# Optimization experiments

Measured on AMD Instinct MI355X. Metric: run time of the kernel, lower is better.

Reference implementation:

```python
import jax, jax.numpy as jnp
import numpy as np

B, T, D, H = 4, 2048, 1024, 16
HD = D // H  # head_dim = 64


def setup_inputs() -> dict:
    key = jax.random.key(0)
    k1, k2, k3 = jax.random.split(key, 3)
    s = 0.02
    return {
        "x": jax.random.normal(k1, (B, T, D), dtype=jnp.float32),
        "qkv_w": jax.random.normal(k2, (D, 3 * D), dtype=jnp.float32) * s,
        "qkv_b": jnp.zeros((3 * D,), dtype=jnp.float32),
        "proj_w": jax.random.normal(k3, (D, D), dtype=jnp.float32) * s,
        "proj_b": jnp.zeros((D,), dtype=jnp.float32),
    }


def reference(x, qkv_w, qkv_b, proj_w, proj_b):
    b, t, d = x.shape
    qkv = x @ qkv_w + qkv_b                       # [B,T,3D]
    q, k, v = jnp.split(qkv, 3, axis=-1)
    # [B,T,D] -> [B,H,T,hd]
    q = q.reshape(b, t, H, HD).transpose(0, 2, 1, 3)
    k = k.reshape(b, t, H, HD).transpose(0, 2, 1, 3)
    v = v.reshape(b, t, H, HD).transpose(0, 2, 1, 3)
    att = jnp.einsum("bhqd,bhkd->bhqk", q, k) / np.sqrt(HD).astype(np.float32)
    causal = jnp.tril(jnp.ones((t, t), dtype=bool))
    att = jnp.where(causal[None, None], att, jnp.finfo(att.dtype).min)
    att = jax.nn.softmax(att, axis=-1)
    out = jnp.einsum("bhqk,bhkd->bhqd", att, v)   # [B,H,T,hd]
    out = out.transpose(0, 2, 1, 3).reshape(b, t, H * HD)
    out = out @ proj_w + proj_b                   # dropout p=0.0 -> identity
    return out
```

## Files before the change

### kernel.cpp

```cpp
#include <hip/hip_runtime.h>
#include <hip/hip_bf16.h>

#define Bsz 4
#define Tsz 2048
#define Dsz 1024
#define Hsz 16
#define HDsz 64

typedef __attribute__((ext_vector_type(8))) __bf16 bf16x8;
typedef __attribute__((ext_vector_type(4))) __bf16 bf16x4;
typedef __attribute__((ext_vector_type(4))) float f32x4;
typedef __attribute__((ext_vector_type(2))) float f32x2;
typedef unsigned short u16;
typedef unsigned int u32;

#define DEVI static __device__ __forceinline__

DEVI u16 f2bf(float f) {
    __bf16 h = (__bf16)f;
    union { __bf16 h; u16 u; } c; c.h = h; return c.u;
}
DEVI bf16x8 ld_bf8(const u16* p) { return *reinterpret_cast<const bf16x8*>(p); }

DEVI void gll16(const u16* g, u16* lds) {
    __builtin_amdgcn_global_load_lds(
        (const __attribute__((address_space(1))) u32*)g,
        (__attribute__((address_space(3))) u32*)lds, 16, 0, 0);
}

DEVI void mfma16(f32x4& c, f32x2 a, f32x2 b) {
    asm("v_mfma_f32_16x16x16_bf16 %0, %1, %2, %0" : "+v"(c) : "v"(a), "v"(b));
}

__global__ __launch_bounds__(256)
void conv_bf16(const float* __restrict__ X, u16* __restrict__ Xb)
{
    const size_t i = ((size_t)blockIdx.x * 256 + threadIdx.x) * 8;
    const float4 a = *(const float4*)(X + i);
    const float4 b = *(const float4*)(X + i + 4);
    u16 h[8] = { f2bf(a.x), f2bf(a.y), f2bf(a.z), f2bf(a.w),
                 f2bf(b.x), f2bf(b.y), f2bf(b.z), f2bf(b.w) };
    *(uint4*)(Xb + i) = *(uint4*)h;
}

__global__ __launch_bounds__(256)
void transpose_w(const float* __restrict__ W, u16* __restrict__ WT, int K, int N)
{
    __shared__ float tile[64][65];
    const int n0 = blockIdx.x * 64, k0 = blockIdx.y * 64;
    const int t = threadIdx.x;
    #pragma unroll
    for (int i = 0; i < 4; ++i) {
        const int idx = i*256 + t;
        const int row = idx >> 4, c4 = (idx & 15) * 4;
        const float4 v = *(const float4*)(W + (size_t)(k0 + row)*N + n0 + c4);
        tile[row][c4+0] = v.x; tile[row][c4+1] = v.y;
        tile[row][c4+2] = v.z; tile[row][c4+3] = v.w;
    }
    __syncthreads();
    #pragma unroll
    for (int j = 0; j < 2; ++j) {
        const int idx = j*256 + t;
        const int nr = idx >> 3, kc = (idx & 7) * 8;
        u16 h[8];
        #pragma unroll
        for (int e = 0; e < 8; ++e) h[e] = f2bf(tile[kc + e][nr]);
        *(uint4*)(WT + (size_t)(n0 + nr)*K + k0 + kc) = *(uint4*)h;
    }
}

template<int EPI>
__global__ __launch_bounds__(256, 3)
void gemm128(const u16* __restrict__ A, const u16* __restrict__ Bt,
             const float* __restrict__ bias, float* __restrict__ Cf,
             u16* __restrict__ Qo, u16* __restrict__ Ko, u16* __restrict__ Vo,
             int M, int N, int K)
{
    __shared__ u16 As[3][128][32];
    __shared__ u16 Bs[3][128][32];

    const int nx  = N >> 7;
    const int q   = nx >> 3;
    const int xcd = blockIdx.x & 7;
    const int c   = blockIdx.x >> 3;
    const int tN  = xcd * q + (q > 1 ? (c % q) : 0);
    const int tM  = (q > 1 ? (c / q) : c);

    const int t = threadIdx.x, l = t & 63, w = t >> 6;
    const int wm = w >> 1, wn = w & 1;
    const int lrow = l & 15, lk = l >> 4;

    f32x4 acc[4][4] = {};

    const u16* Ag = A  + (size_t)tM * 128 * K;
    const u16* Bg = Bt + (size_t)tN * 128 * K;

    int srow[2], sch[2];
    #pragma unroll
    for (int r = 0; r < 2; ++r) {
        const int cc = r*256 + t;
        srow[r] = cc >> 2;
        sch[r]  = (cc & 3) ^ ((srow[r] >> 1) & 3);
    }
    const size_t ldso = (size_t)(t & 192) * 8;

    #define STAGE(buf, ks)                                                      \
        {                                                                       \
            _Pragma("unroll")                                                   \
            for (int r = 0; r < 2; ++r) {                                       \
                gll16(Ag + (size_t)srow[r]*K + (ks) + sch[r]*8,                 \
                      &As[buf][0][0] + (size_t)r*2048 + ldso);                  \
                gll16(Bg + (size_t)srow[r]*K + (ks) + sch[r]*8,                 \
                      &Bs[buf][0][0] + (size_t)r*2048 + ldso);                  \
            }                                                                   \
        }

    STAGE(0, 0);
    STAGE(1, 32);

    const int nk = K >> 5;
    int cur = 0;
    for (int i = 0; i < nk; ++i) {
        if (i + 1 < nk) { asm volatile("s_waitcnt vmcnt(4)" ::: "memory"); }
        else            { asm volatile("s_waitcnt vmcnt(0)" ::: "memory"); }
        __builtin_amdgcn_sched_barrier(0);
        __builtin_amdgcn_s_barrier();

        bf16x8 a[4], bb[4];
        #pragma unroll
        for (int ii = 0; ii < 4; ++ii) {
            const int ar = wm*64 + ii*16 + lrow;
            a[ii] = ld_bf8(&As[cur][ar][(lk ^ ((ar >> 1) & 3)) * 8]);
        }
        #pragma unroll
        for (int j = 0; j < 4; ++j) {
            const int br = wn*64 + j*16 + lrow;
            bb[j] = ld_bf8(&Bs[cur][br][(lk ^ ((br >> 1) & 3)) * 8]);
        }

        if (i + 2 < nk) {
            const int nb = (cur + 2) - ((cur + 2) >= 3 ? 3 : 0);
            STAGE(nb, (i + 2) * 32);
        }

        __builtin_amdgcn_s_setprio(1);
        #pragma unroll
        for (int ii = 0; ii < 4; ++ii)
        #pragma unroll
        for (int j = 0; j < 4; ++j)
            acc[ii][j] = __builtin_amdgcn_mfma_f32_16x16x32_bf16(a[ii], bb[j], acc[ii][j], 0, 0, 0);
        __builtin_amdgcn_s_setprio(0);

        cur = (cur + 1) - ((cur + 1) >= 3 ? 3 : 0);
    }
    #undef STAGE

    #pragma unroll
    for (int i = 0; i < 4; ++i)
    #pragma unroll
    for (int j = 0; j < 4; ++j) {
        const int row0 = tM*128 + wm*64 + i*16 + lk*4;
        const int col  = tN*128 + wn*64 + j*16 + lrow;
        const float bv = bias[col];
        if (EPI == 0) {
            #pragma unroll
            for (int r = 0; r < 4; ++r)
                Cf[(size_t)(row0 + r) * N + col] = acc[i][j][r] + bv;
        } else {
            const int which = col >> 10;
            const int h  = (col & 1023) >> 6;
            const int hd = col & 63;
            if (which == 2) {
                const int b  = row0 >> 11;
                const int tt = row0 & 2047;
                const int bh = b * Hsz + h;
                u16 pk[4] = { f2bf(acc[i][j][0] + bv), f2bf(acc[i][j][1] + bv),
                              f2bf(acc[i][j][2] + bv), f2bf(acc[i][j][3] + bv) };
                *(ushort4*)(Vo + ((size_t)bh * HDsz + hd) * Tsz + tt) = *(ushort4*)pk;
            } else {
                u16* P = (which == 0) ? Qo : Ko;
                #pragma unroll
                for (int r = 0; r < 4; ++r) {
                    const int row = row0 + r;
                    const int bh  = (row >> 11) * Hsz + h;
                    P[((size_t)bh * Tsz + (row & 2047)) * HDsz + hd] =
                        f2bf(acc[i][j][r] + bv);
                }
            }
        }
    }
}

__global__ __launch_bounds__(256, 4)
void attn3(const u16* __restrict__ Q, const u16* __restrict__ K,
           const u16* __restrict__ Vt, u16* __restrict__ AO)
{
    __shared__ u16 KV[2][2][64][64];

    const int y = blockIdx.y;
    const int x = blockIdx.x;
    const int idx = (x + (y >> 4)) & 15;
    const int qt = (idx & 1) ? (idx >> 1) : (15 - (idx >> 1));
    const int bh = y;
    const int t = threadIdx.x, w = t >> 6, l = t & 63;
    const int lrow = l & 15, lk = l >> 4;
    const int qw = qt*128 + w*32;
    const int qwmax = qw + 31;
    const int swz = lrow & 7;

    const u16* Qh = Q  + (size_t)bh * Tsz * HDsz;
    const u16* Kh = K  + (size_t)bh * Tsz * HDsz;
    const u16* Vh = Vt + (size_t)bh * HDsz * Tsz;

    bf16x8 qf[2][2];
    #pragma unroll
    for (int f = 0; f < 2; ++f)
    #pragma unroll
    for (int kh = 0; kh < 2; ++kh)
        qf[f][kh] = ld_bf8(&Qh[(size_t)(qw + f*16 + lrow)*HDsz + kh*32 + lk*8]);

    f32x4 o[2][4] = {};
    float m[2] = {-3e38f, -3e38f}, lsum[2] = {0.f, 0.f};

    const int ntile = 2*qt + 2;
    int cur = 0;

    #pragma unroll
    for (int rr = 0; rr < 2; ++rr) {
        const int c = rr*256 + t;
        const int row = c >> 3, gc = (c & 7) ^ (row & 7);
        gll16(Kh + (size_t)row*HDsz + gc*8,
              &KV[0][0][0][0] + (size_t)(rr*256 + (t & 192))*8);
        gll16(Vh + (size_t)row*Tsz + gc*8,
              &KV[0][1][0][0] + (size_t)(rr*256 + (t & 192))*8);
    }
    __syncthreads();

    for (int tk = 0; tk < ntile; ++tk) {
        if (tk + 1 < ntile) {
            const int nkv = (tk + 1) * 64;
            #pragma unroll
            for (int rr = 0; rr < 2; ++rr) {
                const int c = rr*256 + t;
                const int row = c >> 3, gc = (c & 7) ^ (row & 7);
                gll16(Kh + (size_t)(nkv + row)*HDsz + gc*8,
                      &KV[cur^1][0][0][0] + (size_t)(rr*256 + (t & 192))*8);
                gll16(Vh + (size_t)row*Tsz + nkv + gc*8,
                      &KV[cur^1][1][0][0] + (size_t)(rr*256 + (t & 192))*8);
            }
        }
        const int kv0 = tk * 64;
        if (kv0 <= qwmax) {
            const u16 (*Ks)[64] = KV[cur][0];
            const u16 (*Vs)[64] = KV[cur][1];
            const bool fullc    = (kv0 + 63 <= qwmax);
            const bool needmask = (kv0 + 63 > qw);

            f32x4 s[2][4];
            __builtin_amdgcn_s_setprio(1);
            #pragma unroll
            for (int c = 0; c < 4; ++c) {
                if (c >= 2 && !fullc) continue;
                const bf16x8 k0 = ld_bf8(&Ks[c*16 + lrow][((0 + lk) ^ swz) * 8]);
                const bf16x8 k1 = ld_bf8(&Ks[c*16 + lrow][((4 + lk) ^ swz) * 8]);
                #pragma unroll
                for (int f = 0; f < 2; ++f) {
                    f32x4 z = {};
                    z = __builtin_amdgcn_mfma_f32_16x16x32_bf16(k0, qf[f][0], z, 0, 0, 0);
                    z = __builtin_amdgcn_mfma_f32_16x16x32_bf16(k1, qf[f][1], z, 0, 0, 0);
                    s[f][c] = z;
                }
            }
            __builtin_amdgcn_s_setprio(0);

            #pragma unroll
            for (int f = 0; f < 2; ++f) {
                const int q = qw + f*16 + lrow;
                if (needmask) {
                    #pragma unroll
                    for (int c = 0; c < 4; ++c) {
                        if (c >= 2 && !fullc) continue;
                        const int base = kv0 + c*16 + lk*4;
                        #pragma unroll
                        for (int r = 0; r < 4; ++r)
                            if (base + r > q) s[f][c][r] = -1e30f;
                    }
                }
                f32x4 t01;
                #pragma unroll
                for (int r = 0; r < 4; ++r) {
                    t01[r] = fmaxf(s[f][0][r], s[f][1][r]);
                    if (fullc) t01[r] = fmaxf(t01[r], fmaxf(s[f][2][r], s[f][3][r]));
                }
                float mx = fmaxf(fmaxf(t01[0], t01[1]), fmaxf(t01[2], t01[3]));
                mx = fmaxf(mx, __shfl_xor(mx, 16));
                mx = fmaxf(mx, __shfl_xor(mx, 32));
                if (__any(mx > m[f] + 64.f)) {
                    const float mn = fmaxf(m[f], mx);
                    const float al = __expf((m[f] - mn) * 0.125f);
                    lsum[f] *= al;
                    m[f] = mn;
                    #pragma unroll
                    for (int c = 0; c < 4; ++c)
                    #pragma unroll
                    for (int r = 0; r < 4; ++r) o[f][c][r] *= al;
                }
                const float nm8 = -m[f] * 0.125f;
                f32x4 ps4 = {};
                #pragma unroll
                for (int c = 0; c < 4; ++c) {
                    if (c >= 2 && !fullc) continue;
                    #pragma unroll
                    for (int r = 0; r < 4; ++r) {
                        const float p = __expf(fmaf(s[f][c][r], 0.125f, nm8));
                        s[f][c][r] = p;
                        ps4[r] += p;
                    }
                }
                float ps = (ps4[0] + ps4[1]) + (ps4[2] + ps4[3]);
                ps += __shfl_xor(ps, 16);
                ps += __shfl_xor(ps, 32);
                lsum[f] += ps;
            }

            __builtin_amdgcn_s_setprio(1);
            #pragma unroll
            for (int c = 0; c < 4; ++c) {
                if (c >= 2 && !fullc) continue;
                union { bf16x4 v; f32x2 f; } p0, p1;
                #pragma unroll
                for (int r = 0; r < 4; ++r) {
                    p0.v[r] = (__bf16)s[0][c][r];
                    p1.v[r] = (__bf16)s[1][c][r];
                }
                #pragma unroll
                for (int chd = 0; chd < 4; ++chd) {
                    const f32x2 va = *reinterpret_cast<const f32x2*>(
                        &Vs[chd*16 + lrow][(((c*2 + (lk >> 1)) ^ swz) << 3) + ((lk & 1) << 2)]);
                    mfma16(o[0][chd], va, p0.f);
                    mfma16(o[1][chd], va, p1.f);
                }
            }
            __builtin_amdgcn_s_setprio(0);
        }
        __syncthreads();
        cur ^= 1;
    }

    const int b = bh >> 4, h = bh & 15;
    #pragma unroll
    for (int f = 0; f < 2; ++f) {
        const float rl = 1.0f / lsum[f];
        #pragma unroll
        for (int chd = 0; chd < 4; ++chd) {
            u16 ov[4] = { f2bf(o[f][chd][0]*rl), f2bf(o[f][chd][1]*rl),
                          f2bf(o[f][chd][2]*rl), f2bf(o[f][chd][3]*rl) };
            *(ushort4*)(AO + ((size_t)(b*Tsz + qw + f*16 + lrow))*Dsz
                           + h*HDsz + chd*16 + lk*4) = *(ushort4*)ov;
        }
    }
}

extern "C" void kernel_launch(void* const* d_in, const int* in_sizes, int n_in,
                              void* d_out, int out_size, void* d_ws, size_t ws_size,
                              hipStream_t stream)
{
    (void)in_sizes; (void)n_in; (void)out_size; (void)ws_size;

    const float* x      = (const float*)d_in[0];
    const float* qkv_w  = (const float*)d_in[1];
    const float* qkv_b  = (const float*)d_in[2];
    const float* proj_w = (const float*)d_in[3];
    const float* proj_b = (const float*)d_in[4];
    float* out = (float*)d_out;

    char* ws = (char*)d_ws;
    const size_t SZ = (size_t)Bsz * Hsz * Tsz * HDsz * sizeof(u16);
    u16* R0 = (u16*)(ws);
    u16* Qb = (u16*)(ws + SZ);
    u16* Kb = (u16*)(ws + 2*SZ);
    u16* Vt = (u16*)(ws + 3*SZ);
    u16* WQKVT = R0;
    u16* AO    = R0;
    u16* WPT   = Qb;

    u16* Xb = (u16*)d_out;

    const int M = Bsz * Tsz;

    conv_bf16<<<(M*Dsz)/(256*8), 256, 0, stream>>>(x, Xb);
    transpose_w<<<dim3(3*Dsz/64, Dsz/64), 256, 0, stream>>>(qkv_w, WQKVT, Dsz, 3*Dsz);
    gemm128<1><<<dim3((3*Dsz/128) * (M/128)), 256, 0, stream>>>(
        Xb, WQKVT, qkv_b, nullptr, Qb, Kb, Vt, M, 3*Dsz, Dsz);
    attn3<<<dim3(Tsz/128, Bsz*Hsz), 256, 0, stream>>>(Qb, Kb, Vt, AO);
    transpose_w<<<dim3(Dsz/64, Dsz/64), 256, 0, stream>>>(proj_w, WPT, Dsz, Dsz);
    gemm128<0><<<dim3((Dsz/128) * (M/128)), 256, 0, stream>>>(
        AO, WPT, proj_b, out, nullptr, nullptr, nullptr, M, Dsz, Dsz);
}
```

Baseline: 194.4 us.

## Triple-buffer K/V tiles in attention with one barrier per iteration

The attention kernel moves from a double-buffered K/V LDS ring to a triple-buffered one, prefetching two tiles ahead. It waits with explicit vmcnt counters and takes a single barrier per iteration in place of the trailing __syncthreads. The goal is to hide global-load latency and cut synchronisation stalls. In exchange LDS use per block grows from 32 KB to 48 KB and the occupancy hint drops from 4 to 3 blocks per CU. Correctness now depends on hand-counted vmcnt values matching the number of outstanding loads.

```diff
diff --git a/kernel.cpp b/kernel.cpp
--- a/kernel.cpp
+++ b/kernel.cpp
@@ -191,11 +191,11 @@
     }
 }
 
-__global__ __launch_bounds__(256, 4)
-void attn3(const u16* __restrict__ Q, const u16* __restrict__ K,
+__global__ __launch_bounds__(256, 3)
+void attn6(const u16* __restrict__ Q, const u16* __restrict__ K,
            const u16* __restrict__ Vt, u16* __restrict__ AO)
 {
-    __shared__ u16 KV[2][2][64][64];
+    __shared__ u16 KV[3][2][64][64];
 
     const int y = blockIdx.y;
     const int x = blockIdx.x;
@@ -218,37 +218,42 @@
     #pragma unroll
     for (int kh = 0; kh < 2; ++kh)
         qf[f][kh] = ld_bf8(&Qh[(size_t)(qw + f*16 + lrow)*HDsz + kh*32 + lk*8]);
+    asm volatile("s_waitcnt vmcnt(0)" ::: "memory");
 
     f32x4 o[2][4] = {};
     float m[2] = {-3e38f, -3e38f}, lsum[2] = {0.f, 0.f};
 
     const int ntile = 2*qt + 2;
+
+    #define AST(buf, tkv)                                                       \
+        {                                                                       \
+            const int nkv_ = (tkv) * 64;                                        \
+            _Pragma("unroll")                                                   \
+            for (int rr = 0; rr < 2; ++rr) {                                    \
+                const int c_ = rr*256 + t;                                      \
+                const int row_ = c_ >> 3, gc_ = (c_ & 7) ^ (row_ & 7);          \
+                gll16(Kh + (size_t)(nkv_ + row_)*HDsz + gc_*8,                  \
+                      &KV[buf][0][0][0] + (size_t)(rr*256 + (t & 192))*8);      \
+                gll16(Vh + (size_t)row_*Tsz + nkv_ + gc_*8,                     \
+                      &KV[buf][1][0][0] + (size_t)(rr*256 + (t & 192))*8);      \
+            }                                                                   \
+        }
+
+    AST(0, 0)
+    AST(1, 1)
+
     int cur = 0;
-
-    #pragma unroll
-    for (int rr = 0; rr < 2; ++rr) {
-        const int c = rr*256 + t;
-        const int row = c >> 3, gc = (c & 7) ^ (row & 7);
-        gll16(Kh + (size_t)row*HDsz + gc*8,
-              &KV[0][0][0][0] + (size_t)(rr*256 + (t & 192))*8);
-        gll16(Vh + (size_t)row*Tsz + gc*8,
-              &KV[0][1][0][0] + (size_t)(rr*256 + (t & 192))*8);
-    }
-    __syncthreads();
-
     for (int tk = 0; tk < ntile; ++tk) {
-        if (tk + 1 < ntile) {
-            const int nkv = (tk + 1) * 64;
-            #pragma unroll
-            for (int rr = 0; rr < 2; ++rr) {
-                const int c = rr*256 + t;
-                const int row = c >> 3, gc = (c & 7) ^ (row & 7);
-                gll16(Kh + (size_t)(nkv + row)*HDsz + gc*8,
-                      &KV[cur^1][0][0][0] + (size_t)(rr*256 + (t & 192))*8);
-                gll16(Vh + (size_t)row*Tsz + nkv + gc*8,
-                      &KV[cur^1][1][0][0] + (size_t)(rr*256 + (t & 192))*8);
-            }
-        }
+        if (tk + 1 < ntile) { asm volatile("s_waitcnt vmcnt(4)" ::: "memory"); }
+        else                { asm volatile("s_waitcnt vmcnt(0)" ::: "memory"); }
+        __builtin_amdgcn_sched_barrier(0);
+        __builtin_amdgcn_s_barrier();
+
+        if (tk + 2 < ntile) {
+            const int nb = (cur + 2) - ((cur + 2) >= 3 ? 3 : 0);
+            AST(nb, tk + 2)
+        }
+
         const int kv0 = tk * 64;
         if (kv0 <= qwmax) {
             const u16 (*Ks)[64] = KV[cur][0];
@@ -343,9 +348,9 @@
             }
             __builtin_amdgcn_s_setprio(0);
         }
-        __syncthreads();
-        cur ^= 1;
-    }
+        cur = (cur + 1) - ((cur + 1) >= 3 ? 3 : 0);
+    }
+    #undef AST
 
     const int b = bh >> 4, h = bh & 15;
     #pragma unroll
@@ -392,7 +397,7 @@
     transpose_w<<<dim3(3*Dsz/64, Dsz/64), 256, 0, stream>>>(qkv_w, WQKVT, Dsz, 3*Dsz);
     gemm128<1><<<dim3((3*Dsz/128) * (M/128)), 256, 0, stream>>>(
         Xb, WQKVT, qkv_b, nullptr, Qb, Kb, Vt, M, 3*Dsz, Dsz);
-    attn3<<<dim3(Tsz/128, Bsz*Hsz), 256, 0, stream>>>(Qb, Kb, Vt, AO);
+    attn6<<<dim3(Tsz/128, Bsz*Hsz), 256, 0, stream>>>(Qb, Kb, Vt, AO);
     transpose_w<<<dim3(Dsz/64, Dsz/64), 256, 0, stream>>>(proj_w, WPT, Dsz, Dsz);
     gemm128<0><<<dim3((Dsz/128) * (M/128)), 256, 0, stream>>>(
         AO, WPT, proj_b, out, nullptr, nullptr, nullptr, M, Dsz, Dsz);
```

After: 203.0 us. 4.4% more time.
